# Optimization experiments

Measured on AMD Instinct MI355X. Metric: run time of the kernel, lower is better.

The kernel has to match this reference:

```python
import jax, jax.numpy as jnp
import numpy as np
from functools import partial

# CUBA LIF/LI constants (mock-mode software integration, hxtorch conventions)
DT = 1e-6
TAU_MEM_INV = 1.0 / 6e-6   # dt*tau_mem_inv = 1/6 per-step membrane coupling
TAU_SYN_INV = 1.0 / 6e-6   # dt*tau_syn_inv = 1/6 per-step synaptic decay
ALPHA = 50.0               # SuperSpike surrogate steepness
V_TH = 1.0                 # threshold; leak = reset = 0


@partial(jax.custom_vjp, nondiff_argnums=(1,))
def spike_fn(x, alpha):
    # Heaviside forward, SuperSpike surrogate backward.
    return (x > 0.0).astype(x.dtype)

def _spike_fwd(x, alpha):
    return spike_fn(x, alpha), x

def _spike_bwd(alpha, x, g):
    return (g / (alpha * jnp.abs(x) + 1.0) ** 2,)

spike_fn.defvjp(_spike_fwd, _spike_bwd)


def cuba_lif(inp):
    """CUBA LIF integration over time. inp: [T, B, N] synaptic input; returns spikes [T, B, N]."""
    B, N = inp.shape[1], inp.shape[2]
    v0 = jnp.zeros((B, N), inp.dtype)
    i0 = jnp.zeros((B, N), inp.dtype)

    def step(carry, x):
        v, i = carry
        v = v + DT * TAU_MEM_INV * (-v + i)          # membrane update (leak=0)
        i = i * (1.0 - DT * TAU_SYN_INV) + x          # synaptic current decay + input
        z = spike_fn(v - V_TH, ALPHA)                 # spike
        v = (1.0 - jax.lax.stop_gradient(z)) * v      # reset to 0 (detached spike)
        return (v, i), z

    _, z = jax.lax.scan(step, (v0, i0), inp)
    return z


def cuba_li(inp):
    """CUBA LI (non-spiking readout) integration. inp: [T, B, N]; returns membrane trace [T, B, N]."""
    B, N = inp.shape[1], inp.shape[2]
    v0 = jnp.zeros((B, N), inp.dtype)
    i0 = jnp.zeros((B, N), inp.dtype)

    def step(carry, x):
        v, i = carry
        v = v + DT * TAU_MEM_INV * (-v + i)
        i = i * (1.0 - DT * TAU_SYN_INV) + x
        return (v, i), v

    _, v = jax.lax.scan(step, (v0, i0), inp)
    return v


def setup_inputs() -> dict:
    key = jax.random.key(0)
    k1, k2, k3 = jax.random.split(key, 3)
    T, B, N_IN, N_HID, N_OUT = 256, 128, 784, 512, 128
    spikes = (jax.random.uniform(k1, (T, B, N_IN)) < 0.1).astype(jnp.float32)
    w_hidden = 0.2 * jax.random.normal(k2, (N_HID, N_IN), dtype=jnp.float32)
    w_out = 0.2 * jax.random.normal(k3, (N_OUT, N_HID), dtype=jnp.float32)
    return {"spikes": spikes, "w_hidden": w_hidden, "w_out": w_out}


def reference(spikes, w_hidden, w_out):
    # input_repetitions=1 -> repeat is a no-op. Synapses have no bias.
    c_h = jnp.einsum('tbi,hi->tbh', spikes, w_hidden)   # [T, B, n_hidden]
    s_h = cuba_lif(c_h)                                  # hidden spikes
    c_o = jnp.einsum('tbh,oh->tbo', s_h, w_out)          # [T, B, n_out]
    return cuba_li(c_o)                                  # readout membrane trace (v_cadc)
```

## Files before the change

### kernel.cpp

```cpp
#include <hip/hip_runtime.h>

typedef _Float16 f16;
typedef _Float16 f16x8 __attribute__((ext_vector_type(8)));
typedef float f32x4 __attribute__((ext_vector_type(4)));

#define GLOBAL_AS __attribute__((address_space(1)))
#define LDS_AS __attribute__((address_space(3)))

__device__ __forceinline__ void async16(const void* g, void* l) {
  __builtin_amdgcn_global_load_lds((const GLOBAL_AS unsigned int*)g,
                                   (LDS_AS unsigned int*)l, 16, 0, 0);
}


__global__ __launch_bounds__(256) void conv_a(const float* __restrict__ s,
                                              f16* __restrict__ a16) {
  int idx = blockIdx.x * 256 + threadIdx.x;
  int m = idx / 100;
  int g = idx - m * 100;
  f16x8 h = {};
  if (g < 98) {
    const float4* p = (const float4*)(s + (size_t)m * 784 + g * 8);
    float4 x = p[0];
    float4 y = p[1];
    h[0] = (f16)x.x; h[1] = (f16)x.y; h[2] = (f16)x.z; h[3] = (f16)x.w;
    h[4] = (f16)y.x; h[5] = (f16)y.y; h[6] = (f16)y.z; h[7] = (f16)y.w;
  }
  *(f16x8*)(a16 + (size_t)m * 800 + g * 8) = h;
}

__global__ __launch_bounds__(256) void conv_w(const float* __restrict__ wh,
                                              const float* __restrict__ wo,
                                              f16* __restrict__ w2h,
                                              f16* __restrict__ w2o) {
  int idx = blockIdx.x * 256 + threadIdx.x;
  if (idx < 819200) {
    int h = idx / 1600;
    int c = idx - h * 1600;
    f16 o = (f16)0.f;
    if (c < 784) {
      o = (f16)wh[h * 784 + c];
    } else if (c >= 800 && c < 1584) {
      float x = wh[h * 784 + (c - 800)];
      f16 hi = (f16)x;
      o = (f16)((x - (float)hi) * 2048.0f);
    }
    w2h[idx] = o;
  } else if (idx < 819200 + 65536) {
    int j = idx - 819200;
    w2o[j] = (f16)wo[j];
  }
}

template <int N_LD, int A_STRIDE, int B_STRIDE, int NCH64, bool TAIL32,
          int B_OFF_LO, int KSPLIT_SPAN>
__global__ __launch_bounds__(256, 2) void gemm_f16(const f16* __restrict__ A,
                                                   const f16* __restrict__ B,
                                                   float* __restrict__ C) {
  constexpr bool HAS_LO = (B_OFF_LO > 0);
  __shared__ f16 lds_a[128 * 64];
  __shared__ f16 lds_bh[128 * 64];
  __shared__ f16 lds_bl[HAS_LO ? 128 * 64 : 8];
  const int t = threadIdx.x;
  const int lane = t & 63;
  const int wave = t >> 6;
  const int m0 = blockIdx.y * 128;
  const int n0 = KSPLIT_SPAN ? 0 : blockIdx.x * 128;
  const int kb = KSPLIT_SPAN ? blockIdx.x * KSPLIT_SPAN : 0;
  float* Cp = KSPLIT_SPAN ? C + (size_t)blockIdx.x * 32768 * N_LD : C;
  const int wm = (wave >> 1) * 64;
  const int wn = (wave & 1) * 64;
  const int row = lane & 15;
  const int quad = lane >> 4;

  f32x4 acch[4][4] = {};
  f32x4 accl[HAS_LO ? 4 : 1][4] = {};

  for (int c = 0; c < NCH64; ++c) {
    const int k0 = kb + c * 64;
#pragma unroll
    for (int s = 0; s < 4; ++s) {
      const int j = t + s * 256;
      const int r = j >> 3, g = (j & 7) * 8;
      async16(A + (m0 + r) * A_STRIDE + k0 + g, &lds_a[j * 8]);
      async16(B + (n0 + r) * B_STRIDE + k0 + g, &lds_bh[j * 8]);
      if (HAS_LO) async16(B + (n0 + r) * B_STRIDE + B_OFF_LO + k0 + g, &lds_bl[j * 8]);
    }
    __syncthreads();
#pragma unroll
    for (int ks = 0; ks < 2; ++ks) {
      f16x8 af[4], bh[4], bl[4];
#pragma unroll
      for (int tm = 0; tm < 4; ++tm)
        af[tm] = *(const f16x8*)&lds_a[(wm + tm * 16 + row) * 64 + ks * 32 + quad * 8];
#pragma unroll
      for (int tn = 0; tn < 4; ++tn) {
        bh[tn] = *(const f16x8*)&lds_bh[(wn + tn * 16 + row) * 64 + ks * 32 + quad * 8];
        if (HAS_LO)
          bl[tn] = *(const f16x8*)&lds_bl[(wn + tn * 16 + row) * 64 + ks * 32 + quad * 8];
      }
#pragma unroll
      for (int tm = 0; tm < 4; ++tm)
#pragma unroll
        for (int tn = 0; tn < 4; ++tn) {
          acch[tm][tn] =
              __builtin_amdgcn_mfma_f32_16x16x32_f16(af[tm], bh[tn], acch[tm][tn], 0, 0, 0);
          if (HAS_LO)
            accl[tm][tn] =
                __builtin_amdgcn_mfma_f32_16x16x32_f16(af[tm], bl[tn], accl[tm][tn], 0, 0, 0);
        }
    }
    __syncthreads();
  }

  if (TAIL32) {
    const int k0 = kb + NCH64 * 64;
#pragma unroll
    for (int s = 0; s < 2; ++s) {
      const int j = t + s * 256;
      const int r = j >> 2, g = (j & 3) * 8;
      async16(A + (m0 + r) * A_STRIDE + k0 + g, &lds_a[j * 8]);
      async16(B + (n0 + r) * B_STRIDE + k0 + g, &lds_bh[j * 8]);
      if (HAS_LO) async16(B + (n0 + r) * B_STRIDE + B_OFF_LO + k0 + g, &lds_bl[j * 8]);
    }
    __syncthreads();
    f16x8 af[4], bh[4], bl[4];
#pragma unroll
    for (int tm = 0; tm < 4; ++tm)
      af[tm] = *(const f16x8*)&lds_a[(wm + tm * 16 + row) * 32 + quad * 8];
#pragma unroll
    for (int tn = 0; tn < 4; ++tn) {
      bh[tn] = *(const f16x8*)&lds_bh[(wn + tn * 16 + row) * 32 + quad * 8];
      if (HAS_LO) bl[tn] = *(const f16x8*)&lds_bl[(wn + tn * 16 + row) * 32 + quad * 8];
    }
#pragma unroll
    for (int tm = 0; tm < 4; ++tm)
#pragma unroll
      for (int tn = 0; tn < 4; ++tn) {
        acch[tm][tn] =
            __builtin_amdgcn_mfma_f32_16x16x32_f16(af[tm], bh[tn], acch[tm][tn], 0, 0, 0);
        if (HAS_LO)
          accl[tm][tn] =
              __builtin_amdgcn_mfma_f32_16x16x32_f16(af[tm], bl[tn], accl[tm][tn], 0, 0, 0);
      }
  }

#pragma unroll
  for (int tm = 0; tm < 4; ++tm)
#pragma unroll
    for (int tn = 0; tn < 4; ++tn)
#pragma unroll
      for (int r = 0; r < 4; ++r) {
        const int mm = m0 + wm + tm * 16 + quad * 4 + r;
        const int nn = n0 + wn + tn * 16 + row;
        float val = acch[tm][tn][r];
        if (HAS_LO) val += 4.8828125e-4f * accl[tm][tn][r];
        Cp[(size_t)mm * N_LD + nn] = val;
      }
}

__global__ __launch_bounds__(256) void lif_scan(const float* __restrict__ ch,
                                                f16* __restrict__ sh) {
  const int n = blockIdx.x * 256 + threadIdx.x;
  float xa[8], xb[8];
#pragma unroll
  for (int j = 0; j < 8; ++j) xa[j] = ch[j * 65536 + n];
  float v = 0.f, cur = 0.f;
  for (int c = 0; c < 32; ++c) {
    const int nc = (c + 1) & 31;
#pragma unroll
    for (int j = 0; j < 8; ++j) xb[j] = ch[(nc * 8 + j) * 65536 + n];
#pragma unroll
    for (int j = 0; j < 8; ++j) {
      const int t = c * 8 + j;
      float x = xa[j];
      v = v + 0.16666667f * (cur - v);
      cur = 0.8333333f * cur + x;
      bool z = v > 1.0f;
      sh[t * 65536 + n] = z ? (f16)1.f : (f16)0.f;
      v = z ? 0.f : v;
    }
#pragma unroll
    for (int j = 0; j < 8; ++j) xa[j] = xb[j];
  }
}

__global__ __launch_bounds__(64) void li_scan(const float* __restrict__ coA,
                                              const float* __restrict__ coB,
                                              float* __restrict__ out) {
  const int n = blockIdx.x * 64 + threadIdx.x;
  float xa[8], xb[8];
#pragma unroll
  for (int j = 0; j < 8; ++j) xa[j] = coA[j * 16384 + n] + coB[j * 16384 + n];
  float v = 0.f, cur = 0.f;
  for (int c = 0; c < 32; ++c) {
    const int nc = (c + 1) & 31;
#pragma unroll
    for (int j = 0; j < 8; ++j)
      xb[j] = coA[(nc * 8 + j) * 16384 + n] + coB[(nc * 8 + j) * 16384 + n];
#pragma unroll
    for (int j = 0; j < 8; ++j) {
      const int t = c * 8 + j;
      v = v + 0.16666667f * (cur - xa[j] * 0.f - v);
      cur = 0.8333333f * cur + xa[j];
      out[t * 16384 + n] = v;
    }
#pragma unroll
    for (int j = 0; j < 8; ++j) xa[j] = xb[j];
  }
}

extern "C" void kernel_launch(void* const* d_in, const int* in_sizes, int n_in,
                              void* d_out, int out_size, void* d_ws, size_t ws_size,
                              hipStream_t stream) {
  const float* spikes = (const float*)d_in[0];
  const float* w_hidden = (const float*)d_in[1];
  const float* w_out = (const float*)d_in[2];
  float* out = (float*)d_out;

  char* ws = (char*)d_ws;
  f16* A16 = (f16*)ws;
  float* coA = (float*)ws;
  float* coB = (float*)(ws + 16777216);
  f16* w2h = (f16*)(ws + 52428800);
  float* c_h = (float*)(ws + 52428800 + 1638400);
  f16* s_h = (f16*)(ws + 52428800 + 1638400 + 67108864);
  f16* w2o = (f16*)(ws + 52428800 + 1638400 + 67108864 + 33554432);

  conv_a<<<12800, 256, 0, stream>>>(spikes, A16);
  conv_w<<<3456, 256, 0, stream>>>(w_hidden, w_out, w2h, w2o);

  gemm_f16<512, 800, 1600, 12, true, 800, 0>
      <<<dim3(4, 256), 256, 0, stream>>>(A16, w2h, c_h);

  lif_scan<<<256, 256, 0, stream>>>(c_h, s_h);

  gemm_f16<128, 512, 512, 4, false, 0, 256>
      <<<dim3(2, 256), 256, 0, stream>>>(s_h, w2o, coA);

  li_scan<<<256, 64, 0, stream>>>(coA, coB, out);
}
```

Before: 267.5 us.

## Swizzle GEMM LDS layout, remap blocks across XCDs, segment LI scan with warmup

The GEMM now stores tiles in LDS with an XOR swizzle on the 16-byte column group, so the fragment reads for the MFMA inputs avoid bank conflicts. The first GEMM switches to a 1D grid whose block index is remapped so that blocks on the same XCD share A rows and B columns in L2. The LI readout scan is split into four 64-step time segments run by separate threads. Each later segment replays the preceding 64 steps from zero state as warmup, relying on the 5/6 and 1/6 decay to make the truncated history negligible. This trades exact recurrence and some redundant reads for 4x more parallel threads.

```diff
diff --git a/kernel.cpp b/kernel.cpp
--- a/kernel.cpp
+++ b/kernel.cpp
@@ -53,7 +53,7 @@
 }
 
 template <int N_LD, int A_STRIDE, int B_STRIDE, int NCH64, bool TAIL32,
-          int B_OFF_LO, int KSPLIT_SPAN>
+          int B_OFF_LO, int KSPLIT_SPAN, bool XCD_SWZ>
 __global__ __launch_bounds__(256, 2) void gemm_f16(const f16* __restrict__ A,
                                                    const f16* __restrict__ B,
                                                    float* __restrict__ C) {
@@ -64,10 +64,19 @@
   const int t = threadIdx.x;
   const int lane = t & 63;
   const int wave = t >> 6;
-  const int m0 = blockIdx.y * 128;
-  const int n0 = KSPLIT_SPAN ? 0 : blockIdx.x * 128;
-  const int kb = KSPLIT_SPAN ? blockIdx.x * KSPLIT_SPAN : 0;
-  float* Cp = KSPLIT_SPAN ? C + (size_t)blockIdx.x * 32768 * N_LD : C;
+  int bx, by;
+  if (XCD_SWZ) {
+    const int b = blockIdx.x;
+    by = (b & 7) + 8 * (b >> 5);
+    bx = (b >> 3) & 3;
+  } else {
+    bx = blockIdx.x;
+    by = blockIdx.y;
+  }
+  const int m0 = by * 128;
+  const int n0 = KSPLIT_SPAN ? 0 : bx * 128;
+  const int kb = KSPLIT_SPAN ? bx * KSPLIT_SPAN : 0;
+  float* Cp = KSPLIT_SPAN ? C + (size_t)bx * 32768 * N_LD : C;
   const int wm = (wave >> 1) * 64;
   const int wn = (wave & 1) * 64;
   const int row = lane & 15;
@@ -81,23 +90,29 @@
 #pragma unroll
     for (int s = 0; s < 4; ++s) {
       const int j = t + s * 256;
-      const int r = j >> 3, g = (j & 7) * 8;
-      async16(A + (m0 + r) * A_STRIDE + k0 + g, &lds_a[j * 8]);
-      async16(B + (n0 + r) * B_STRIDE + k0 + g, &lds_bh[j * 8]);
-      if (HAS_LO) async16(B + (n0 + r) * B_STRIDE + B_OFF_LO + k0 + g, &lds_bl[j * 8]);
+      const int r = j >> 3;
+      const int g = (j & 7) ^ (r & 7);
+      async16(A + (m0 + r) * A_STRIDE + k0 + g * 8, &lds_a[j * 8]);
+      async16(B + (n0 + r) * B_STRIDE + k0 + g * 8, &lds_bh[j * 8]);
+      if (HAS_LO)
+        async16(B + (n0 + r) * B_STRIDE + B_OFF_LO + k0 + g * 8, &lds_bl[j * 8]);
     }
     __syncthreads();
 #pragma unroll
     for (int ks = 0; ks < 2; ++ks) {
       f16x8 af[4], bh[4], bl[4];
 #pragma unroll
-      for (int tm = 0; tm < 4; ++tm)
-        af[tm] = *(const f16x8*)&lds_a[(wm + tm * 16 + row) * 64 + ks * 32 + quad * 8];
+      for (int tm = 0; tm < 4; ++tm) {
+        const int ra = wm + tm * 16 + row;
+        const int p = (ks * 4 + quad) ^ (ra & 7);
+        af[tm] = *(const f16x8*)&lds_a[ra * 64 + p * 8];
+      }
 #pragma unroll
       for (int tn = 0; tn < 4; ++tn) {
-        bh[tn] = *(const f16x8*)&lds_bh[(wn + tn * 16 + row) * 64 + ks * 32 + quad * 8];
-        if (HAS_LO)
-          bl[tn] = *(const f16x8*)&lds_bl[(wn + tn * 16 + row) * 64 + ks * 32 + quad * 8];
+        const int rb = wn + tn * 16 + row;
+        const int p = (ks * 4 + quad) ^ (rb & 7);
+        bh[tn] = *(const f16x8*)&lds_bh[rb * 64 + p * 8];
+        if (HAS_LO) bl[tn] = *(const f16x8*)&lds_bl[rb * 64 + p * 8];
       }
 #pragma unroll
       for (int tm = 0; tm < 4; ++tm)
@@ -118,20 +133,27 @@
 #pragma unroll
     for (int s = 0; s < 2; ++s) {
       const int j = t + s * 256;
-      const int r = j >> 2, g = (j & 3) * 8;
-      async16(A + (m0 + r) * A_STRIDE + k0 + g, &lds_a[j * 8]);
-      async16(B + (n0 + r) * B_STRIDE + k0 + g, &lds_bh[j * 8]);
-      if (HAS_LO) async16(B + (n0 + r) * B_STRIDE + B_OFF_LO + k0 + g, &lds_bl[j * 8]);
+      const int r = j >> 2;
+      const int g = (j & 3) ^ (r & 3);
+      async16(A + (m0 + r) * A_STRIDE + k0 + g * 8, &lds_a[j * 8]);
+      async16(B + (n0 + r) * B_STRIDE + k0 + g * 8, &lds_bh[j * 8]);
+      if (HAS_LO)
+        async16(B + (n0 + r) * B_STRIDE + B_OFF_LO + k0 + g * 8, &lds_bl[j * 8]);
     }
     __syncthreads();
     f16x8 af[4], bh[4], bl[4];
 #pragma unroll
-    for (int tm = 0; tm < 4; ++tm)
-      af[tm] = *(const f16x8*)&lds_a[(wm + tm * 16 + row) * 32 + quad * 8];
+    for (int tm = 0; tm < 4; ++tm) {
+      const int ra = wm + tm * 16 + row;
+      const int p = quad ^ (ra & 3);
+      af[tm] = *(const f16x8*)&lds_a[ra * 32 + p * 8];
+    }
 #pragma unroll
     for (int tn = 0; tn < 4; ++tn) {
-      bh[tn] = *(const f16x8*)&lds_bh[(wn + tn * 16 + row) * 32 + quad * 8];
-      if (HAS_LO) bl[tn] = *(const f16x8*)&lds_bl[(wn + tn * 16 + row) * 32 + quad * 8];
+      const int rb = wn + tn * 16 + row;
+      const int p = quad ^ (rb & 3);
+      bh[tn] = *(const f16x8*)&lds_bh[rb * 32 + p * 8];
+      if (HAS_LO) bl[tn] = *(const f16x8*)&lds_bl[rb * 32 + p * 8];
     }
 #pragma unroll
     for (int tm = 0; tm < 4; ++tm)
@@ -185,23 +207,48 @@
   }
 }
 
-__global__ __launch_bounds__(64) void li_scan(const float* __restrict__ coA,
-                                              const float* __restrict__ coB,
-                                              float* __restrict__ out) {
-  const int n = blockIdx.x * 64 + threadIdx.x;
+__global__ __launch_bounds__(256) void li_scan_seg(const float* __restrict__ coA,
+                                                   const float* __restrict__ coB,
+                                                   float* __restrict__ out) {
+  const int tid = blockIdx.x * 256 + threadIdx.x;
+  const int n = tid & 16383;
+  const int seg = tid >> 14;
+  const int t0 = seg * 64;
+  float v = 0.f, cur = 0.f;
   float xa[8], xb[8];
-#pragma unroll
-  for (int j = 0; j < 8; ++j) xa[j] = coA[j * 16384 + n] + coB[j * 16384 + n];
-  float v = 0.f, cur = 0.f;
-  for (int c = 0; c < 32; ++c) {
-    const int nc = (c + 1) & 31;
+  if (seg) {
+    const int w0 = t0 - 64;
 #pragma unroll
     for (int j = 0; j < 8; ++j)
-      xb[j] = coA[(nc * 8 + j) * 16384 + n] + coB[(nc * 8 + j) * 16384 + n];
+      xa[j] = coA[(w0 + j) * 16384 + n] + coB[(w0 + j) * 16384 + n];
+    for (int c = 0; c < 8; ++c) {
+      const int nb = w0 + (c + 1) * 8;
+#pragma unroll
+      for (int j = 0; j < 8; ++j)
+        xb[j] = coA[(nb + j) * 16384 + n] + coB[(nb + j) * 16384 + n];
+#pragma unroll
+      for (int j = 0; j < 8; ++j) {
+        v = v + 0.16666667f * (cur - v);
+        cur = 0.8333333f * cur + xa[j];
+      }
+#pragma unroll
+      for (int j = 0; j < 8; ++j) xa[j] = xb[j];
+    }
+  } else {
+#pragma unroll
+    for (int j = 0; j < 8; ++j) xa[j] = coA[j * 16384 + n] + coB[j * 16384 + n];
+  }
+  for (int c = 0; c < 8; ++c) {
+    if (c < 7) {
+      const int nb = t0 + (c + 1) * 8;
+#pragma unroll
+      for (int j = 0; j < 8; ++j)
+        xb[j] = coA[(nb + j) * 16384 + n] + coB[(nb + j) * 16384 + n];
+    }
 #pragma unroll
     for (int j = 0; j < 8; ++j) {
-      const int t = c * 8 + j;
-      v = v + 0.16666667f * (cur - xa[j] * 0.f - v);
+      const int t = t0 + c * 8 + j;
+      v = v + 0.16666667f * (cur - v);
       cur = 0.8333333f * cur + xa[j];
       out[t * 16384 + n] = v;
     }
@@ -230,13 +277,13 @@
   conv_a<<<12800, 256, 0, stream>>>(spikes, A16);
   conv_w<<<3456, 256, 0, stream>>>(w_hidden, w_out, w2h, w2o);
 
-  gemm_f16<512, 800, 1600, 12, true, 800, 0>
-      <<<dim3(4, 256), 256, 0, stream>>>(A16, w2h, c_h);
+  gemm_f16<512, 800, 1600, 12, true, 800, 0, true>
+      <<<1024, 256, 0, stream>>>(A16, w2h, c_h);
 
   lif_scan<<<256, 256, 0, stream>>>(c_h, s_h);
 
-  gemm_f16<128, 512, 512, 4, false, 0, 256>
+  gemm_f16<128, 512, 512, 4, false, 0, 256, false>
       <<<dim3(2, 256), 256, 0, stream>>>(s_h, w2o, coA);
 
-  li_scan<<<256, 64, 0, stream>>>(coA, coB, out);
-}
+  li_scan_seg<<<256, 256, 0, stream>>>(coA, coB, out);
+}
```

After: 251.5 us. 6.0% less time.
